# Kernel tuning notes

Hardware: AMD Instinct MI355X
Metric: run time of the kernel (lower is better)

## Reference

```python
import jax, jax.numpy as jnp
import numpy as np

B, S, E, H, R = 512, 50, 128, 8, 32
D = E // H  # depth per head
USERS, ITEMS, ALLSEQ, NCLASS = 50000, 20000, 20000, 5


def setup_inputs() -> dict:
    key = jax.random.key(0)
    ks = jax.random.split(key, 20)
    n = lambda k, shp, s=0.05: jax.random.normal(k, shp, dtype=jnp.float32) * s
    return {
        "user": jax.random.randint(ks[0], (B,), 0, USERS),
        "item": jax.random.randint(ks[1], (B,), 0, ITEMS),
        "neighbor": jax.random.randint(ks[2], (B, S), 0, USERS),
        "seq": jax.random.randint(ks[3], (B, S), 0, ALLSEQ),
        "user_emb_table": n(ks[4], (USERS, E)),
        "item_emb_table": n(ks[5], (ITEMS, E)),
        "user_item_LCU": n(ks[6], (ALLSEQ, R, E), 0.01),
        "item_user_LCU": n(ks[7], (ALLSEQ, R, E), 0.01),
        "wq": n(ks[8], (E, E)), "bq": jnp.zeros((E,), jnp.float32),
        "wk": n(ks[9], (E, E)), "bk": jnp.zeros((E,), jnp.float32),
        "wv": n(ks[10], (E, E)), "bv": jnp.zeros((E,), jnp.float32),
        "wo": n(ks[11], (E, E)), "bo": jnp.zeros((E,), jnp.float32),
        "fc_w": n(ks[12], (R, NCLASS)), "fc_b": jnp.zeros((NCLASS,), jnp.float32),
    }


def _forward(user, item, neighbor, seq,
             user_emb_table, item_emb_table, user_item_LCU, item_user_LCU,
             wq, bq, wk, bk, wv, bv, wo, bo, fc_w, fc_b):
    user_emb = user_emb_table[user]            # [B,E]
    neighbor_emb = user_emb_table[neighbor]    # [B,S,E]
    item_emb = item_emb_table[item]            # [B,E]
    weight = (neighbor > 0).astype(jnp.float32)  # [B,S] padding mask (1=real)

    # ---- single-query multi-head attention (use_attention=True) ----
    q = (user_emb @ wq + bq).reshape(B, H, D)                       # [B,H,D]
    k = (neighbor_emb @ wk + bk).reshape(B, S, H, D).transpose(0, 2, 1, 3)  # [B,H,S,D]
    v = (neighbor_emb @ wv + bv).reshape(B, S, H, D).transpose(0, 2, 1, 3)  # [B,H,S,D]
    logits = jnp.einsum('bhd,bhsd->bhs', q, k) / jnp.sqrt(jnp.float32(D))
    logits = logits + (1.0 - weight)[:, None, :] * (-1e9)           # mask padding
    attn = jax.nn.softmax(logits, axis=-1)                          # [B,H,S]
    ctx = attn[..., None] * v                                       # [B,H,S,D]
    ctx = ctx.transpose(0, 2, 1, 3).reshape(B, S, E)                # [B,S,E]
    neighbor_emb = ctx @ wo + bo                                    # [B,S,E]

    # ---- region embedding ----
    K_ui = user_item_LCU[seq]   # [B,S,R,E]
    K_iu = item_user_LCU[seq]   # [B,S,R,E]
    neighbor_profile = jnp.einsum('bsre,bse->bsr', K_iu, neighbor_emb)  # [B,S,R]
    item_profile = jnp.einsum('bsre,be->bsr', K_ui, item_emb)          # [B,S,R]
    neighbor_rating = neighbor_profile * item_profile * weight[:, :, None]
    user_rating_vector = jnp.max(neighbor_rating, axis=1)              # [B,R]

    # ---- rating classifier ----
    return jax.nn.softmax(user_rating_vector @ fc_w + fc_b, axis=-1)   # [B,NCLASS]


def reference(user, item, neighbor, seq,
              user_emb_table, item_emb_table, user_item_LCU, item_user_LCU,
              wq, bq, wk, bk, wv, bv, wo, bo, fc_w, fc_b):
    return _forward(user, item, neighbor, seq,
                    user_emb_table, item_emb_table, user_item_LCU, item_user_LCU,
                    wq, bq, wk, bk, wv, bv, wo, bo, fc_w, fc_b)
```

## Files before the change

kernel.cpp:

```cpp
#include <hip/hip_runtime.h>
#include <math.h>

#define BB 512
#define SS 50
#define EE 128
#define HH 8
#define RR 32
#define NC 5
#define NSEQ 20000
#define NBS (BB*SS)
#define LDK 136

typedef __attribute__((ext_vector_type(8))) __bf16 bf16x8;
typedef __attribute__((ext_vector_type(4))) float f32x4;
typedef __attribute__((ext_vector_type(4))) unsigned short us4;

__device__ __forceinline__ unsigned short f2bf(float f) {
    unsigned int u = __float_as_uint(f);
    unsigned int r = (u + 0x7fffu + ((u >> 16) & 1u)) >> 16;
    return (unsigned short)r;
}
__device__ __forceinline__ float dot4v(const f32x4& a, const float4& b) {
    return a[0]*b.x + a[1]*b.y + a[2]*b.z + a[3]*b.w;
}

__global__ __launch_bounds__(256) void prep_kernel(const float* __restrict__ wv,
                                                   const float* __restrict__ wo,
                                                   unsigned short* __restrict__ wvT,
                                                   unsigned short* __restrict__ woT,
                                                   const int* __restrict__ seq,
                                                   int* __restrict__ hist) {
    const int bid = blockIdx.x, t = threadIdx.x;
    if (bid < 128) {
        const int n = bid;
        if (t < 128) wvT[n*EE + t] = f2bf(wv[t*EE + n]);
        else         woT[n*EE + (t - 128)] = f2bf(wo[(t - 128)*EE + n]);
    } else {
        const int i = (bid - 128) * 256 + t;
        if (i < NBS) atomicAdd(&hist[seq[i]], 1);
    }
}

__global__ __launch_bounds__(1024) void scan_kernel(int* __restrict__ hist,
                                                    int* __restrict__ hstart) {
    const int t = threadIdx.x;
    const int CH = 20;
    const int base = t * CH;
    int loc[CH];
    int s = 0;
    #pragma unroll
    for (int i = 0; i < CH; ++i) {
        int idx = base + i;
        int v = (idx < NSEQ) ? hist[idx] : 0;
        loc[i] = s; s += v;
    }
    const int lane = t & 63, w = t >> 6;
    int incl = s;
    #pragma unroll
    for (int off = 1; off < 64; off <<= 1) {
        int n = __shfl_up(incl, off);
        if (lane >= off) incl += n;
    }
    __shared__ int wsum[16];
    if (lane == 63) wsum[w] = incl;
    __syncthreads();
    if (t == 0) {
        int acc = 0;
        #pragma unroll
        for (int k = 0; k < 16; ++k) { int v = wsum[k]; wsum[k] = acc; acc += v; }
    }
    __syncthreads();
    const int excl = incl - s + wsum[w];
    #pragma unroll
    for (int i = 0; i < CH; ++i) {
        int idx = base + i;
        if (idx < NSEQ) {
            int e = excl + loc[i];
            hist[idx] = e;
            hstart[idx] = e;
        }
    }
    if (t == 0) hstart[NSEQ] = NBS;
}

__global__ __launch_bounds__(256) void scatter_kernel(const int* __restrict__ seq,
                                                      int* __restrict__ hist,
                                                      int* __restrict__ perm) {
    int i = blockIdx.x * 256 + threadIdx.x;
    if (i < NBS) {
        int pos = atomicAdd(&hist[seq[i]], 1);
        perm[pos] = i;
    }
}

__global__ __launch_bounds__(256, 4) void attn_kernel(
    const int* __restrict__ user,
    const int* __restrict__ neighbor,
    const float* __restrict__ uet,
    const float* __restrict__ wq, const float* __restrict__ bq,
    const float* __restrict__ wk, const float* __restrict__ bk,
    const float* __restrict__ bv, const float* __restrict__ bo,
    const unsigned short* __restrict__ wvT, const unsigned short* __restrict__ woT,
    float* __restrict__ ws_ne2)
{
    __shared__ unsigned short kA[64*LDK];
    __shared__ unsigned short qkvT[16][EE];
    __shared__ float ue[EE];
    __shared__ float qs[EE];
    __shared__ float qkb[HH];
    __shared__ float attn_s[HH][64];
    __shared__ float maskadd[64];

    const int b = blockIdx.x;
    const int t = threadIdx.x;

    if (t < EE) ue[t] = uet[(size_t)user[b]*EE + t];
    if (t < 64) maskadd[t] = (t < SS && neighbor[b*SS + t] > 0) ? 0.f : -1e9f;
    for (int idx = t; idx < SS*32; idx += 256) {
        int s = idx >> 5, g = idx & 31;
        float4 v = ((const float4*)(uet + (size_t)neighbor[b*SS + s]*EE))[g];
        us4 o; o.x = f2bf(v.x); o.y = f2bf(v.y); o.z = f2bf(v.z); o.w = f2bf(v.w);
        *(us4*)&kA[s*LDK + g*4] = o;
    }
    for (int idx = t; idx < 14*LDK; idx += 256) kA[50*LDK + idx] = 0;
    for (int idx = t; idx < 8*EE; idx += 256) qkvT[8 + (idx >> 7)][idx & 127] = 0;
    __syncthreads();

    if (t < EE) {
        float acc = bq[t];
        #pragma unroll 4
        for (int e = 0; e < EE; ++e) acc = fmaf(ue[e], wq[e*EE + t], acc);
        qs[t] = acc;
    }
    __syncthreads();

    {
        const int e = t >> 1, h0 = (t & 1) * 4;
        const float* wrow = wk + e*EE;
        #pragma unroll
        for (int j = 0; j < 4; ++j) {
            int h = h0 + j;
            float acc = 0.f;
            #pragma unroll
            for (int d = 0; d < 16; ++d) acc = fmaf(qs[h*16 + d], wrow[h*16 + d], acc);
            qkvT[h][e] = f2bf(acc);
        }
    }
    if (t < HH) {
        float acc = 0.f;
        #pragma unroll
        for (int d = 0; d < 16; ++d) acc = fmaf(qs[t*16 + d], bk[t*16 + d], acc);
        qkb[t] = acc;
    }
    __syncthreads();

    const int w    = t >> 6;
    const int l    = t & 63;
    const int lrow = l & 15;
    const int kg   = l >> 4;

    bf16x8 a0 = *(const bf16x8*)&kA[(w*16 + lrow)*LDK +  0 + kg*8];
    bf16x8 a1 = *(const bf16x8*)&kA[(w*16 + lrow)*LDK + 32 + kg*8];
    bf16x8 a2 = *(const bf16x8*)&kA[(w*16 + lrow)*LDK + 64 + kg*8];
    bf16x8 a3 = *(const bf16x8*)&kA[(w*16 + lrow)*LDK + 96 + kg*8];

    {
        bf16x8 b0 = *(const bf16x8*)&qkvT[lrow][ 0 + kg*8];
        bf16x8 b1 = *(const bf16x8*)&qkvT[lrow][32 + kg*8];
        bf16x8 b2 = *(const bf16x8*)&qkvT[lrow][64 + kg*8];
        bf16x8 b3 = *(const bf16x8*)&qkvT[lrow][96 + kg*8];
        f32x4 c = {0.f, 0.f, 0.f, 0.f};
        c = __builtin_amdgcn_mfma_f32_16x16x32_bf16(a0, b0, c, 0, 0, 0);
        c = __builtin_amdgcn_mfma_f32_16x16x32_bf16(a1, b1, c, 0, 0, 0);
        c = __builtin_amdgcn_mfma_f32_16x16x32_bf16(a2, b2, c, 0, 0, 0);
        c = __builtin_amdgcn_mfma_f32_16x16x32_bf16(a3, b3, c, 0, 0, 0);
        const int h = lrow;
        if (h < HH) {
            #pragma unroll
            for (int rg = 0; rg < 4; ++rg) {
                const int row = w*16 + kg*4 + rg;
                attn_s[h][row] = (c[rg] + qkb[h]) * 0.25f + maskadd[row];
            }
        }
    }
    __syncthreads();

    if (t < 64) {
        int h = t >> 3, ll = t & 7;
        float mx = -3e38f;
        #pragma unroll
        for (int i = 0; i < 7; ++i) { int s = i*8 + ll; if (s < SS) mx = fmaxf(mx, attn_s[h][s]); }
        mx = fmaxf(mx, __shfl_xor(mx, 1));
        mx = fmaxf(mx, __shfl_xor(mx, 2));
        mx = fmaxf(mx, __shfl_xor(mx, 4));
        float ev[7]; float sm_ = 0.f;
        #pragma unroll
        for (int i = 0; i < 7; ++i) {
            int s = i*8 + ll; ev[i] = 0.f;
            if (s < SS) { ev[i] = expf(attn_s[h][s] - mx); sm_ += ev[i]; }
        }
        sm_ += __shfl_xor(sm_, 1);
        sm_ += __shfl_xor(sm_, 2);
        sm_ += __shfl_xor(sm_, 4);
        float inv = 1.f / sm_;
        #pragma unroll
        for (int i = 0; i < 7; ++i) { int s = i*8 + ll; if (s < SS) attn_s[h][s] = ev[i] * inv; }
    }
    __syncthreads();

    f32x4 acc[8];
    #pragma unroll
    for (int nt = 0; nt < 8; ++nt) {
        const unsigned short* bp = wvT + (nt*16 + lrow)*EE + kg*8;
        bf16x8 b0 = *(const bf16x8*)&bp[0];
        bf16x8 b1 = *(const bf16x8*)&bp[32];
        bf16x8 b2 = *(const bf16x8*)&bp[64];
        bf16x8 b3 = *(const bf16x8*)&bp[96];
        f32x4 c = {0.f, 0.f, 0.f, 0.f};
        c = __builtin_amdgcn_mfma_f32_16x16x32_bf16(a0, b0, c, 0, 0, 0);
        c = __builtin_amdgcn_mfma_f32_16x16x32_bf16(a1, b1, c, 0, 0, 0);
        c = __builtin_amdgcn_mfma_f32_16x16x32_bf16(a2, b2, c, 0, 0, 0);
        c = __builtin_amdgcn_mfma_f32_16x16x32_bf16(a3, b3, c, 0, 0, 0);
        acc[nt] = c;
    }
    #pragma unroll
    for (int nt = 0; nt < 8; ++nt) {
        const int col = nt*16 + lrow;
        const float bvc = bv[col];
        #pragma unroll
        for (int rg = 0; rg < 4; ++rg) {
            const int row = w*16 + kg*4 + rg;
            const float av = (row < SS) ? attn_s[nt][row] : 0.f;
            kA[row*LDK + col] = f2bf((acc[nt][rg] + bvc) * av);
        }
    }
    __syncthreads();

    bf16x8 c0 = *(const bf16x8*)&kA[(w*16 + lrow)*LDK +  0 + kg*8];
    bf16x8 c1 = *(const bf16x8*)&kA[(w*16 + lrow)*LDK + 32 + kg*8];
    bf16x8 c2 = *(const bf16x8*)&kA[(w*16 + lrow)*LDK + 64 + kg*8];
    bf16x8 c3 = *(const bf16x8*)&kA[(w*16 + lrow)*LDK + 96 + kg*8];

    #pragma unroll
    for (int nt = 0; nt < 8; ++nt) {
        const unsigned short* bp = woT + (nt*16 + lrow)*EE + kg*8;
        bf16x8 b0 = *(const bf16x8*)&bp[0];
        bf16x8 b1 = *(const bf16x8*)&bp[32];
        bf16x8 b2 = *(const bf16x8*)&bp[64];
        bf16x8 b3 = *(const bf16x8*)&bp[96];
        f32x4 c = {0.f, 0.f, 0.f, 0.f};
        c = __builtin_amdgcn_mfma_f32_16x16x32_bf16(c0, b0, c, 0, 0, 0);
        c = __builtin_amdgcn_mfma_f32_16x16x32_bf16(c1, b1, c, 0, 0, 0);
        c = __builtin_amdgcn_mfma_f32_16x16x32_bf16(c2, b2, c, 0, 0, 0);
        c = __builtin_amdgcn_mfma_f32_16x16x32_bf16(c3, b3, c, 0, 0, 0);
        const int col = nt*16 + lrow;
        const float boc = bo[col];
        #pragma unroll
        for (int rg = 0; rg < 4; ++rg) {
            const int row = w*16 + kg*4 + rg;
            if (row < SS)
                ws_ne2[((size_t)b*SS + row)*EE + col] = c[rg] + boc;
        }
    }
}

__global__ __launch_bounds__(256) void region_kernel(
    const int* __restrict__ neighbor, const int* __restrict__ item,
    const float* __restrict__ ui_lcu, const float* __restrict__ iu_lcu,
    const float* __restrict__ iet, const float* __restrict__ ws_ne2,
    const int* __restrict__ hstart, const int* __restrict__ perm,
    float* __restrict__ ws_np, float* __restrict__ ws_ip)
{
    const int bid = blockIdx.x;
    const bool ip_half = (bid >= NSEQ);
    const int j = ip_half ? (bid - NSEQ) : bid;
    const int start = hstart[j];
    const int end   = hstart[j + 1];
    if (start >= end) return;

    const int t = threadIdx.x;
    const int r = t >> 3, l = t & 7;

    const float* tab = ip_half ? ui_lcu : iu_lcu;
    const f32x4* kg = (const f32x4*)(tab + ((size_t)j*RR + r)*EE);
    f32x4 k0 = kg[l], k1 = kg[l + 8], k2 = kg[l + 16], k3 = kg[l + 24];

    if (ip_half) {
        for (int o = start; o < end; ++o) {
            const int bs = perm[o];
            const int b  = (unsigned)bs / SS;
            const float4* v4 = (const float4*)(iet + (size_t)item[b]*EE);
            float acc = dot4v(k0, v4[l]) + dot4v(k1, v4[l + 8])
                      + dot4v(k2, v4[l + 16]) + dot4v(k3, v4[l + 24]);
            acc += __shfl_xor(acc, 1); acc += __shfl_xor(acc, 2); acc += __shfl_xor(acc, 4);
            if (l == 0) ws_ip[(size_t)bs*RR + r] = acc;
        }
    } else {
        for (int o = start; o < end; ++o) {
            const int bs = perm[o];
            const float4* v4 = (const float4*)(ws_ne2 + (size_t)bs*EE);
            float acc = dot4v(k0, v4[l]) + dot4v(k1, v4[l + 8])
                      + dot4v(k2, v4[l + 16]) + dot4v(k3, v4[l + 24]);
            acc += __shfl_xor(acc, 1); acc += __shfl_xor(acc, 2); acc += __shfl_xor(acc, 4);
            if (l == 0) {
                const float w = (neighbor[bs] > 0) ? 1.f : 0.f;
                ws_np[(size_t)bs*RR + r] = acc * w;
            }
        }
    }
}

__global__ __launch_bounds__(256) void head_kernel(
    const float* __restrict__ ws_np, const float* __restrict__ ws_ip,
    const float* __restrict__ fc_w, const float* __restrict__ fc_b,
    float* __restrict__ out)
{
    __shared__ float part[8][RR];
    __shared__ float urv[RR];
    __shared__ float lg[NC];
    const int b = blockIdx.x, t = threadIdx.x;
    const int r = t & 31, sub = t >> 5;

    float m = -3e38f;
    for (int s = sub; s < SS; s += 8) {
        const size_t idx = ((size_t)b*SS + s)*RR + r;
        m = fmaxf(m, ws_np[idx] * ws_ip[idx]);
    }
    part[sub][r] = m;
    __syncthreads();
    if (t < RR) {
        float mm = part[0][t];
        #pragma unroll
        for (int k = 1; k < 8; ++k) mm = fmaxf(mm, part[k][t]);
        urv[t] = mm;
    }
    __syncthreads();
    if (t < NC) {
        float acc = fc_b[t];
        #pragma unroll
        for (int rr = 0; rr < RR; ++rr) acc = fmaf(urv[rr], fc_w[rr*NC + t], acc);
        lg[t] = acc;
    }
    __syncthreads();
    if (t < NC) {
        float mx = lg[0];
        #pragma unroll
        for (int c = 1; c < NC; ++c) mx = fmaxf(mx, lg[c]);
        float sm = 0.f;
        #pragma unroll
        for (int c = 0; c < NC; ++c) sm += expf(lg[c] - mx);
        out[b*NC + t] = expf(lg[t] - mx) / sm;
    }
}

extern "C" void kernel_launch(void* const* d_in, const int* in_sizes, int n_in,
                              void* d_out, int out_size, void* d_ws, size_t ws_size,
                              hipStream_t stream) {
    const int*   user     = (const int*)d_in[0];
    const int*   item     = (const int*)d_in[1];
    const int*   neighbor = (const int*)d_in[2];
    const int*   seq      = (const int*)d_in[3];
    const float* uet      = (const float*)d_in[4];
    const float* iet      = (const float*)d_in[5];
    const float* ui_lcu   = (const float*)d_in[6];
    const float* iu_lcu   = (const float*)d_in[7];
    const float* wq = (const float*)d_in[8];   const float* bq = (const float*)d_in[9];
    const float* wk = (const float*)d_in[10];  const float* bk = (const float*)d_in[11];
    const float* wv = (const float*)d_in[12];  const float* bv = (const float*)d_in[13];
    const float* wo = (const float*)d_in[14];  const float* bo = (const float*)d_in[15];
    const float* fcw = (const float*)d_in[16]; const float* fcb = (const float*)d_in[17];

    float* ws = (float*)d_ws;
    float* ws_ne2 = ws;
    float* ws_np  = ws_ne2 + (size_t)BB*SS*EE;
    float* ws_ip  = ws_np  + (size_t)BB*SS*RR;
    unsigned short* wvT = (unsigned short*)(ws_ip + (size_t)BB*SS*RR);
    unsigned short* woT = wvT + EE*EE;
    int*   hist   = (int*)(woT + EE*EE);
    int*   hstart = hist + NSEQ;
    int*   perm   = hstart + NSEQ + 1;
    float* out = (float*)d_out;

    hipMemsetAsync(hist, 0, NSEQ * sizeof(int), stream);
    hipLaunchKernelGGL(prep_kernel, dim3(128 + (NBS + 255)/256), dim3(256), 0, stream,
                       wv, wo, wvT, woT, seq, hist);
    hipLaunchKernelGGL(scan_kernel, dim3(1), dim3(1024), 0, stream, hist, hstart);
    hipLaunchKernelGGL(scatter_kernel, dim3((NBS + 255)/256), dim3(256), 0, stream, seq, hist, perm);

    hipLaunchKernelGGL(attn_kernel, dim3(BB), dim3(256), 0, stream,
                       user, neighbor, uet,
                       wq, bq, wk, bk, bv, bo, wvT, woT, ws_ne2);

    hipLaunchKernelGGL(region_kernel, dim3(2*NSEQ), dim3(256), 0, stream,
                       neighbor, item, ui_lcu, iu_lcu, iet, ws_ne2, hstart, perm,
                       ws_np, ws_ip);

    hipLaunchKernelGGL(head_kernel, dim3(BB), dim3(256), 0, stream,
                       ws_np, ws_ip, fcw, fcb, out);
}
```

Before: 182.2 us.

## Compact non-empty seq buckets and grid-stride region kernel with LCU prefetch

The scan now builds a compacted list of non-empty seq buckets and their start offsets. The region kernel runs as a fixed persistent grid of 2048 blocks per half and strides over that list, double-buffering the next bucket's LCU rows in registers while the current bucket is processed. The scatter step packs the padding-mask bit and the item index into per-position arrays, so the region kernel skips those dependent gathers. This targets the cost of launching 40000 mostly idle blocks and exposed LCU load latency, at the price of more registers and a 16-bit bs packing assumption.

```diff
diff --git a/kernel.cpp b/kernel.cpp
--- a/kernel.cpp
+++ b/kernel.cpp
@@ -10,6 +10,7 @@
 #define NSEQ 20000
 #define NBS (BB*SS)
 #define LDK 136
+#define NRB 2048
 
 typedef __attribute__((ext_vector_type(8))) __bf16 bf16x8;
 typedef __attribute__((ext_vector_type(4))) float f32x4;
@@ -42,54 +43,72 @@
 }
 
 __global__ __launch_bounds__(1024) void scan_kernel(int* __restrict__ hist,
-                                                    int* __restrict__ hstart) {
+                                                    int* __restrict__ jlist,
+                                                    int* __restrict__ jstart,
+                                                    int* __restrict__ Mcount) {
     const int t = threadIdx.x;
     const int CH = 20;
     const int base = t * CH;
-    int loc[CH];
-    int s = 0;
+    int val[CH];
+    int s = 0, cz = 0;
     #pragma unroll
     for (int i = 0; i < CH; ++i) {
         int idx = base + i;
         int v = (idx < NSEQ) ? hist[idx] : 0;
-        loc[i] = s; s += v;
+        val[i] = v;
+        s += v;
+        cz += (v > 0) ? 1 : 0;
     }
     const int lane = t & 63, w = t >> 6;
-    int incl = s;
+    int incl = s, incl2 = cz;
     #pragma unroll
     for (int off = 1; off < 64; off <<= 1) {
-        int n = __shfl_up(incl, off);
-        if (lane >= off) incl += n;
-    }
-    __shared__ int wsum[16];
-    if (lane == 63) wsum[w] = incl;
+        int n1 = __shfl_up(incl, off);
+        int n2 = __shfl_up(incl2, off);
+        if (lane >= off) { incl += n1; incl2 += n2; }
+    }
+    __shared__ int wsum[16], wsum2[16];
+    if (lane == 63) { wsum[w] = incl; wsum2[w] = incl2; }
     __syncthreads();
     if (t == 0) {
-        int acc = 0;
-        #pragma unroll
-        for (int k = 0; k < 16; ++k) { int v = wsum[k]; wsum[k] = acc; acc += v; }
-    }
-    __syncthreads();
-    const int excl = incl - s + wsum[w];
+        int a = 0, b = 0;
+        #pragma unroll
+        for (int k = 0; k < 16; ++k) {
+            int v1 = wsum[k], v2 = wsum2[k];
+            wsum[k] = a; wsum2[k] = b;
+            a += v1; b += v2;
+        }
+    }
+    __syncthreads();
+    int e  = incl  - s  + wsum[w];
+    int c2 = incl2 - cz + wsum2[w];
     #pragma unroll
     for (int i = 0; i < CH; ++i) {
         int idx = base + i;
         if (idx < NSEQ) {
-            int e = excl + loc[i];
             hist[idx] = e;
-            hstart[idx] = e;
-        }
-    }
-    if (t == 0) hstart[NSEQ] = NBS;
+            if (val[i] > 0) { jlist[c2] = idx; jstart[c2] = e; ++c2; }
+            e += val[i];
+        }
+    }
+    if (t == 1023) {
+        int M = wsum2[15] + incl2;
+        Mcount[0] = M;
+        jstart[M] = NBS;
+    }
 }
 
 __global__ __launch_bounds__(256) void scatter_kernel(const int* __restrict__ seq,
+                                                      const int* __restrict__ neighbor,
+                                                      const int* __restrict__ item,
                                                       int* __restrict__ hist,
-                                                      int* __restrict__ perm) {
+                                                      int* __restrict__ pinfo,
+                                                      int* __restrict__ pitem) {
     int i = blockIdx.x * 256 + threadIdx.x;
     if (i < NBS) {
         int pos = atomicAdd(&hist[seq[i]], 1);
-        perm[pos] = i;
+        pinfo[pos] = i | ((neighbor[i] > 0) ? 0 : 0x80000000);
+        pitem[pos] = item[(unsigned)i / SS];
     }
 }
 
@@ -265,49 +284,80 @@
 }
 
 __global__ __launch_bounds__(256) void region_kernel(
-    const int* __restrict__ neighbor, const int* __restrict__ item,
-    const float* __restrict__ ui_lcu, const float* __restrict__ iu_lcu,
-    const float* __restrict__ iet, const float* __restrict__ ws_ne2,
-    const int* __restrict__ hstart, const int* __restrict__ perm,
+    const float* __restrict__ iu_lcu, const float* __restrict__ ui_lcu,
+    const float* __restrict__ ws_ne2, const float* __restrict__ iet,
+    const int* __restrict__ jlist, const int* __restrict__ jstart,
+    const int* __restrict__ pinfo, const int* __restrict__ pitem,
+    const int* __restrict__ Mcount,
     float* __restrict__ ws_np, float* __restrict__ ws_ip)
 {
-    const int bid = blockIdx.x;
-    const bool ip_half = (bid >= NSEQ);
-    const int j = ip_half ? (bid - NSEQ) : bid;
-    const int start = hstart[j];
-    const int end   = hstart[j + 1];
-    if (start >= end) return;
-
-    const int t = threadIdx.x;
-    const int r = t >> 3, l = t & 7;
-
-    const float* tab = ip_half ? ui_lcu : iu_lcu;
-    const f32x4* kg = (const f32x4*)(tab + ((size_t)j*RR + r)*EE);
-    f32x4 k0 = kg[l], k1 = kg[l + 8], k2 = kg[l + 16], k3 = kg[l + 24];
-
-    if (ip_half) {
-        for (int o = start; o < end; ++o) {
-            const int bs = perm[o];
-            const int b  = (unsigned)bs / SS;
-            const float4* v4 = (const float4*)(iet + (size_t)item[b]*EE);
-            float acc = dot4v(k0, v4[l]) + dot4v(k1, v4[l + 8])
-                      + dot4v(k2, v4[l + 16]) + dot4v(k3, v4[l + 24]);
-            acc += __shfl_xor(acc, 1); acc += __shfl_xor(acc, 2); acc += __shfl_xor(acc, 4);
-            if (l == 0) ws_ip[(size_t)bs*RR + r] = acc;
-        }
-    } else {
-        for (int o = start; o < end; ++o) {
-            const int bs = perm[o];
-            const float4* v4 = (const float4*)(ws_ne2 + (size_t)bs*EE);
-            float acc = dot4v(k0, v4[l]) + dot4v(k1, v4[l + 8])
-                      + dot4v(k2, v4[l + 16]) + dot4v(k3, v4[l + 24]);
-            acc += __shfl_xor(acc, 1); acc += __shfl_xor(acc, 2); acc += __shfl_xor(acc, 4);
-            if (l == 0) {
-                const float w = (neighbor[bs] > 0) ? 1.f : 0.f;
-                ws_np[(size_t)bs*RR + r] = acc * w;
-            }
-        }
-    }
+    const int M = Mcount[0];
+    const int half = blockIdx.x >> 11;
+    int c = blockIdx.x & (NRB - 1);
+    if (c >= M) return;
+
+    const int t = threadIdx.x, r = t >> 3, l = t & 7;
+    const float* lcu  = half ? ui_lcu : iu_lcu;
+    const float* vecs = half ? iet    : ws_ne2;
+    float* outb       = half ? ws_ip  : ws_np;
+
+    f32x4 A0, A1, A2, A3, B0, B1, B2, B3;
+    int sCur, eCur;
+    {
+        int j = jlist[c];
+        sCur = jstart[c]; eCur = jstart[c+1];
+        const f32x4* kp = (const f32x4*)(lcu + ((size_t)j*RR + r)*EE);
+        A0 = kp[l]; A1 = kp[l+8]; A2 = kp[l+16]; A3 = kp[l+24];
+    }
+
+#define DOTSTORE(P0,P1,P2,P3, v0,v1,v2,v3, info_) {                               \
+    float acc_ = dot4v(P0,v0) + dot4v(P1,v1) + dot4v(P2,v2) + dot4v(P3,v3);       \
+    acc_ += __shfl_xor(acc_,1); acc_ += __shfl_xor(acc_,2); acc_ += __shfl_xor(acc_,4); \
+    if (l == 0) {                                                                 \
+        int bs_ = (info_) & 0xFFFF;                                               \
+        outb[(size_t)bs_*RR + r] = half ? acc_ : (((info_) < 0) ? 0.f : acc_);    \
+    } }
+
+#define STAGE(C0,C1,C2,C3, N0,N1,N2,N3) {                                         \
+    const int sC = sCur, eC = eCur, nC = eC - sC;                                 \
+    const int cn = c + NRB;                                                       \
+    const bool more = (cn < M);                                                   \
+    const int jN = more ? jlist[cn] : 0;                                          \
+    sCur = more ? jstart[cn]   : 0;                                               \
+    eCur = more ? jstart[cn+1] : 0;                                               \
+    const int i0 = pinfo[sC];                                                     \
+    const int i1 = (nC >= 2) ? pinfo[sC+1] : i0;                                  \
+    const int t0 = half ? pitem[sC] : (i0 & 0xFFFF);                              \
+    const int t1 = half ? ((nC >= 2) ? pitem[sC+1] : t0) : (i1 & 0xFFFF);         \
+    const float4* rb0 = (const float4*)(vecs + (size_t)t0*EE);                    \
+    float4 r0 = rb0[l], r1 = rb0[l+8], r2 = rb0[l+16], r3 = rb0[l+24];            \
+    float4 s0, s1, s2, s3;                                                        \
+    if (nC >= 2) {                                                                \
+        const float4* rb1 = (const float4*)(vecs + (size_t)t1*EE);                \
+        s0 = rb1[l]; s1 = rb1[l+8]; s2 = rb1[l+16]; s3 = rb1[l+24];               \
+    }                                                                             \
+    if (more) {                                                                   \
+        const f32x4* kp = (const f32x4*)(lcu + ((size_t)jN*RR + r)*EE);           \
+        N0 = kp[l]; N1 = kp[l+8]; N2 = kp[l+16]; N3 = kp[l+24];                   \
+    }                                                                             \
+    DOTSTORE(C0,C1,C2,C3, r0,r1,r2,r3, i0);                                       \
+    if (nC >= 2) DOTSTORE(C0,C1,C2,C3, s0,s1,s2,s3, i1);                          \
+    for (int o = sC + 2; o < eC; ++o) {                                           \
+        const int ii = pinfo[o];                                                  \
+        const int tt = half ? pitem[o] : (ii & 0xFFFF);                           \
+        const float4* rb = (const float4*)(vecs + (size_t)tt*EE);                 \
+        float4 q0 = rb[l], q1 = rb[l+8], q2 = rb[l+16], q3 = rb[l+24];            \
+        DOTSTORE(C0,C1,C2,C3, q0,q1,q2,q3, ii);                                   \
+    }                                                                             \
+    if (!more) break;                                                             \
+    c = cn; }
+
+    while (true) {
+        STAGE(A0,A1,A2,A3, B0,B1,B2,B3)
+        STAGE(B0,B1,B2,B3, A0,A1,A2,A3)
+    }
+#undef STAGE
+#undef DOTSTORE
 }
 
 __global__ __launch_bounds__(256) void head_kernel(
@@ -345,10 +395,10 @@
     if (t < NC) {
         float mx = lg[0];
         #pragma unroll
-        for (int c = 1; c < NC; ++c) mx = fmaxf(mx, lg[c]);
+        for (int cc = 1; cc < NC; ++cc) mx = fmaxf(mx, lg[cc]);
         float sm = 0.f;
         #pragma unroll
-        for (int c = 0; c < NC; ++c) sm += expf(lg[c] - mx);
+        for (int cc = 0; cc < NC; ++cc) sm += expf(lg[cc] - mx);
         out[b*NC + t] = expf(lg[t] - mx) / sm;
     }
 }
@@ -376,24 +426,29 @@
     float* ws_ip  = ws_np  + (size_t)BB*SS*RR;
     unsigned short* wvT = (unsigned short*)(ws_ip + (size_t)BB*SS*RR);
     unsigned short* woT = wvT + EE*EE;
-    int*   hist   = (int*)(woT + EE*EE);
-    int*   hstart = hist + NSEQ;
-    int*   perm   = hstart + NSEQ + 1;
+    int* hist   = (int*)(woT + EE*EE);
+    int* jlist  = hist + NSEQ;
+    int* jstart = jlist + NSEQ;
+    int* Mcount = jstart + NSEQ + 1;
+    int* pinfo  = Mcount + 1;
+    int* pitem  = pinfo + NBS;
     float* out = (float*)d_out;
 
     hipMemsetAsync(hist, 0, NSEQ * sizeof(int), stream);
     hipLaunchKernelGGL(prep_kernel, dim3(128 + (NBS + 255)/256), dim3(256), 0, stream,
                        wv, wo, wvT, woT, seq, hist);
-    hipLaunchKernelGGL(scan_kernel, dim3(1), dim3(1024), 0, stream, hist, hstart);
-    hipLaunchKernelGGL(scatter_kernel, dim3((NBS + 255)/256), dim3(256), 0, stream, seq, hist, perm);
+    hipLaunchKernelGGL(scan_kernel, dim3(1), dim3(1024), 0, stream,
+                       hist, jlist, jstart, Mcount);
+    hipLaunchKernelGGL(scatter_kernel, dim3((NBS + 255)/256), dim3(256), 0, stream,
+                       seq, neighbor, item, hist, pinfo, pitem);
 
     hipLaunchKernelGGL(attn_kernel, dim3(BB), dim3(256), 0, stream,
                        user, neighbor, uet,
                        wq, bq, wk, bk, bv, bo, wvT, woT, ws_ne2);
 
-    hipLaunchKernelGGL(region_kernel, dim3(2*NSEQ), dim3(256), 0, stream,
-                       neighbor, item, ui_lcu, iu_lcu, iet, ws_ne2, hstart, perm,
-                       ws_np, ws_ip);
+    hipLaunchKernelGGL(region_kernel, dim3(2*NRB), dim3(256), 0, stream,
+                       iu_lcu, ui_lcu, ws_ne2, iet,
+                       jlist, jstart, pinfo, pitem, Mcount, ws_np, ws_ip);
 
     hipLaunchKernelGGL(head_kernel, dim3(BB), dim3(256), 0, stream,
                        ws_np, ws_ip, fcw, fcb, out);
```

New measurement: 195.1 us. 7.1% more time.

## Process one sorted (b,s) pair per region block, fusing both LCU projections

Applied to the files above, without the earlier changes.

The region kernel previously launched one block per seq id per table (2*NSEQ blocks), kept the LCU slice in registers and looped serially over all pairs sharing that id. It now launches one block per sorted pair, computing the neighbor and item profiles together. The scatter step precomputes the seq id, the mask bit and the item id per sorted slot, so hstart and perm lookups go away. This removes the serial loops and the many empty blocks, but the LCU rows are reloaded per pair and rely on L2 hits from neighbouring blocks sorted by seq.

```diff
diff --git a/kernel.cpp b/kernel.cpp
--- a/kernel.cpp
+++ b/kernel.cpp
@@ -20,8 +20,8 @@
     unsigned int r = (u + 0x7fffu + ((u >> 16) & 1u)) >> 16;
     return (unsigned short)r;
 }
-__device__ __forceinline__ float dot4v(const f32x4& a, const float4& b) {
-    return a[0]*b.x + a[1]*b.y + a[2]*b.z + a[3]*b.w;
+__device__ __forceinline__ float dot44(const f32x4& a, const f32x4& b) {
+    return a[0]*b[0] + a[1]*b[1] + a[2]*b[2] + a[3]*b[3];
 }
 
 __global__ __launch_bounds__(256) void prep_kernel(const float* __restrict__ wv,
@@ -41,8 +41,7 @@
     }
 }
 
-__global__ __launch_bounds__(1024) void scan_kernel(int* __restrict__ hist,
-                                                    int* __restrict__ hstart) {
+__global__ __launch_bounds__(1024) void scan_kernel(int* __restrict__ hist) {
     const int t = threadIdx.x;
     const int CH = 20;
     const int base = t * CH;
@@ -74,22 +73,24 @@
     #pragma unroll
     for (int i = 0; i < CH; ++i) {
         int idx = base + i;
-        if (idx < NSEQ) {
-            int e = excl + loc[i];
-            hist[idx] = e;
-            hstart[idx] = e;
-        }
-    }
-    if (t == 0) hstart[NSEQ] = NBS;
+        if (idx < NSEQ) hist[idx] = excl + loc[i];
+    }
 }
 
 __global__ __launch_bounds__(256) void scatter_kernel(const int* __restrict__ seq,
+                                                      const int* __restrict__ neighbor,
+                                                      const int* __restrict__ item,
                                                       int* __restrict__ hist,
-                                                      int* __restrict__ perm) {
+                                                      int* __restrict__ pseq,
+                                                      int* __restrict__ pinfo,
+                                                      int* __restrict__ pitem) {
     int i = blockIdx.x * 256 + threadIdx.x;
     if (i < NBS) {
-        int pos = atomicAdd(&hist[seq[i]], 1);
-        perm[pos] = i;
+        const int j = seq[i];
+        int pos = atomicAdd(&hist[j], 1);
+        pseq[pos]  = j;
+        pinfo[pos] = i | ((neighbor[i] > 0) ? 0 : 0x80000000);
+        pitem[pos] = item[(unsigned)i / SS];
     }
 }
 
@@ -264,49 +265,37 @@
     }
 }
 
-__global__ __launch_bounds__(256) void region_kernel(
-    const int* __restrict__ neighbor, const int* __restrict__ item,
-    const float* __restrict__ ui_lcu, const float* __restrict__ iu_lcu,
-    const float* __restrict__ iet, const float* __restrict__ ws_ne2,
-    const int* __restrict__ hstart, const int* __restrict__ perm,
+__global__ __launch_bounds__(256, 6) void region_kernel(
+    const float* __restrict__ iu_lcu, const float* __restrict__ ui_lcu,
+    const float* __restrict__ ws_ne2, const float* __restrict__ iet,
+    const int* __restrict__ pseq, const int* __restrict__ pinfo,
+    const int* __restrict__ pitem,
     float* __restrict__ ws_np, float* __restrict__ ws_ip)
 {
-    const int bid = blockIdx.x;
-    const bool ip_half = (bid >= NSEQ);
-    const int j = ip_half ? (bid - NSEQ) : bid;
-    const int start = hstart[j];
-    const int end   = hstart[j + 1];
-    if (start >= end) return;
-
-    const int t = threadIdx.x;
-    const int r = t >> 3, l = t & 7;
-
-    const float* tab = ip_half ? ui_lcu : iu_lcu;
-    const f32x4* kg = (const f32x4*)(tab + ((size_t)j*RR + r)*EE);
-    f32x4 k0 = kg[l], k1 = kg[l + 8], k2 = kg[l + 16], k3 = kg[l + 24];
-
-    if (ip_half) {
-        for (int o = start; o < end; ++o) {
-            const int bs = perm[o];
-            const int b  = (unsigned)bs / SS;
-            const float4* v4 = (const float4*)(iet + (size_t)item[b]*EE);
-            float acc = dot4v(k0, v4[l]) + dot4v(k1, v4[l + 8])
-                      + dot4v(k2, v4[l + 16]) + dot4v(k3, v4[l + 24]);
-            acc += __shfl_xor(acc, 1); acc += __shfl_xor(acc, 2); acc += __shfl_xor(acc, 4);
-            if (l == 0) ws_ip[(size_t)bs*RR + r] = acc;
-        }
-    } else {
-        for (int o = start; o < end; ++o) {
-            const int bs = perm[o];
-            const float4* v4 = (const float4*)(ws_ne2 + (size_t)bs*EE);
-            float acc = dot4v(k0, v4[l]) + dot4v(k1, v4[l + 8])
-                      + dot4v(k2, v4[l + 16]) + dot4v(k3, v4[l + 24]);
-            acc += __shfl_xor(acc, 1); acc += __shfl_xor(acc, 2); acc += __shfl_xor(acc, 4);
-            if (l == 0) {
-                const float w = (neighbor[bs] > 0) ? 1.f : 0.f;
-                ws_np[(size_t)bs*RR + r] = acc * w;
-            }
-        }
+    const int o = blockIdx.x;
+    const int t = threadIdx.x, r = t >> 3, l = t & 7;
+    const int j    = pseq[o];
+    const int info = pinfo[o];
+    const int bs   = info & 0xFFFF;
+    const int it   = pitem[o];
+
+    const f32x4* kiu = (const f32x4*)(iu_lcu + ((size_t)j*RR + r)*EE);
+    const f32x4* kui = (const f32x4*)(ui_lcu + ((size_t)j*RR + r)*EE);
+    const f32x4* nr  = (const f32x4*)(ws_ne2 + (size_t)bs*EE);
+    const f32x4* ir  = (const f32x4*)(iet + (size_t)it*EE);
+
+    float np = 0.f, ip = 0.f;
+    #pragma unroll
+    for (int i = 0; i < 4; ++i) {
+        const int c = l + 8*i;
+        np += dot44(kiu[c], nr[c]);
+        ip += dot44(kui[c], ir[c]);
+    }
+    np += __shfl_xor(np, 1); np += __shfl_xor(np, 2); np += __shfl_xor(np, 4);
+    ip += __shfl_xor(ip, 1); ip += __shfl_xor(ip, 2); ip += __shfl_xor(ip, 4);
+    if (l == 0) {
+        ws_np[(size_t)bs*RR + r] = (info < 0) ? 0.f : np;
+        ws_ip[(size_t)bs*RR + r] = ip;
     }
 }
 
@@ -345,10 +334,10 @@
     if (t < NC) {
         float mx = lg[0];
         #pragma unroll
-        for (int c = 1; c < NC; ++c) mx = fmaxf(mx, lg[c]);
+        for (int cc = 1; cc < NC; ++cc) mx = fmaxf(mx, lg[cc]);
         float sm = 0.f;
         #pragma unroll
-        for (int c = 0; c < NC; ++c) sm += expf(lg[c] - mx);
+        for (int cc = 0; cc < NC; ++cc) sm += expf(lg[cc] - mx);
         out[b*NC + t] = expf(lg[t] - mx) / sm;
     }
 }
@@ -373,27 +362,29 @@
     float* ws = (float*)d_ws;
     float* ws_ne2 = ws;
     float* ws_np  = ws_ne2 + (size_t)BB*SS*EE;
-    float* ws_ip  = ws_np  + (size_t)BB*SS*RR;
-    unsigned short* wvT = (unsigned short*)(ws_ip + (size_t)BB*SS*RR);
+    float* ws_ip  = ws_np  + (size_t)NBS*RR;
+    unsigned short* wvT = (unsigned short*)(ws_ip + (size_t)NBS*RR);
     unsigned short* woT = wvT + EE*EE;
-    int*   hist   = (int*)(woT + EE*EE);
-    int*   hstart = hist + NSEQ;
-    int*   perm   = hstart + NSEQ + 1;
+    int* hist  = (int*)(woT + EE*EE);
+    int* pseq  = hist + NSEQ;
+    int* pinfo = pseq + NBS;
+    int* pitem = pinfo + NBS;
     float* out = (float*)d_out;
 
     hipMemsetAsync(hist, 0, NSEQ * sizeof(int), stream);
     hipLaunchKernelGGL(prep_kernel, dim3(128 + (NBS + 255)/256), dim3(256), 0, stream,
                        wv, wo, wvT, woT, seq, hist);
-    hipLaunchKernelGGL(scan_kernel, dim3(1), dim3(1024), 0, stream, hist, hstart);
-    hipLaunchKernelGGL(scatter_kernel, dim3((NBS + 255)/256), dim3(256), 0, stream, seq, hist, perm);
+    hipLaunchKernelGGL(scan_kernel, dim3(1), dim3(1024), 0, stream, hist);
+    hipLaunchKernelGGL(scatter_kernel, dim3((NBS + 255)/256), dim3(256), 0, stream,
+                       seq, neighbor, item, hist, pseq, pinfo, pitem);
 
     hipLaunchKernelGGL(attn_kernel, dim3(BB), dim3(256), 0, stream,
                        user, neighbor, uet,
                        wq, bq, wk, bk, bv, bo, wvT, woT, ws_ne2);
 
-    hipLaunchKernelGGL(region_kernel, dim3(2*NSEQ), dim3(256), 0, stream,
-                       neighbor, item, ui_lcu, iu_lcu, iet, ws_ne2, hstart, perm,
-                       ws_np, ws_ip);
+    hipLaunchKernelGGL(region_kernel, dim3(NBS), dim3(256), 0, stream,
+                       iu_lcu, ui_lcu, ws_ne2, iet,
+                       pseq, pinfo, pitem, ws_np, ws_ip);
 
     hipLaunchKernelGGL(head_kernel, dim3(BB), dim3(256), 0, stream,
                        ws_np, ws_ip, fcw, fcb, out);
```

Result: slower. 196.5 us (+7.9%).
